# Kernel optimization log

Measured on AMD Instinct MI355X. Metric: run time of the kernel, lower is better.

## Reference

```python
import jax, jax.numpy as jnp
import numpy as np

N = 100000   # nodes
E = 1600000  # edges (avg degree 16)
DIN, DH, DOUT = 128, 64, 40


def setup_inputs() -> dict:
    key = jax.random.key(0)
    ks = jax.random.split(key, 6)
    x = jax.random.normal(ks[0], (N, DIN), dtype=jnp.float32)
    edge_index = jax.random.randint(ks[1], (2, E), 0, N, dtype=jnp.int32)
    s1 = float(1.0 / np.sqrt(DIN))
    s2 = float(1.0 / np.sqrt(DH))
    W1 = jax.random.uniform(ks[2], (DIN, DH), jnp.float32, -s1, s1)
    b1 = jax.random.uniform(ks[3], (DH,), jnp.float32, -s1, s1)
    W2 = jax.random.uniform(ks[4], (DH, DOUT), jnp.float32, -s2, s2)
    b2 = jax.random.uniform(ks[5], (DOUT,), jnp.float32, -s2, s2)
    return {"x": x, "W1": W1, "b1": b1, "W2": W2, "b2": b2, "edge_index": edge_index}


def _gcn_conv(x, W, b, src, dst):
    """PyG GCNConv: add self-loops, symmetric degree normalization, scatter-add."""
    n = x.shape[0]
    h = x @ W  # [N, F_out] — transform before propagation (PyG order)
    ones = jnp.ones(src.shape[0], dtype=h.dtype)
    deg = jax.ops.segment_sum(ones, dst, num_segments=n) + 1.0  # +1 for self-loop
    dinv = jax.lax.rsqrt(deg)  # deg >= 1, no zero guard needed
    norm = dinv[src] * dinv[dst]  # [E]
    agg = jax.ops.segment_sum(h[src] * norm[:, None], dst, num_segments=n)
    agg = agg + h * (dinv * dinv)[:, None]  # self-loop messages
    return agg + b


def reference(x, W1, b1, W2, b2, edge_index):
    src, dst = edge_index[0], edge_index[1]
    h = jax.nn.relu(_gcn_conv(x, W1, b1, src, dst))
    out = _gcn_conv(h, W2, b2, src, dst)
    return jax.nn.log_softmax(out, axis=1)
```

## Files before the change

kernel.cpp:

```cpp
#include <hip/hip_runtime.h>
#include <hip/hip_fp16.h>
#include <math.h>

#define N_NODES 100000
#define N_EDGES 1600000
#define DIN 128
#define DH 64
#define DOUT 40

#define NB 256
#define BN 391
#define CAP 8192
#define BIN_BLOCKS 512
#define EPB 3125

typedef unsigned short u16;
typedef unsigned int u32;

__device__ inline __half2 u2h(u32 u) {
    union { u32 x; __half2 h; } c; c.x = u; return c.h;
}
__device__ inline u32 h2u(__half2 h) {
    union { __half2 h; u32 x; } c; c.h = h; return c.x;
}


__global__ __launch_bounds__(256) void k_bin(const int* __restrict__ src,
                                             const int* __restrict__ dst,
                                             int* __restrict__ gcur,
                                             u32* __restrict__ staged) {
    __shared__ int hist[NB];
    __shared__ int base[NB];
    __shared__ int cur[NB];
    int t = threadIdx.x;
    for (int i = t; i < NB; i += 256) { hist[i] = 0; cur[i] = 0; }
    __syncthreads();
    int e0 = blockIdx.x * EPB;
    int e1 = e0 + EPB; if (e1 > N_EDGES) e1 = N_EDGES;
    for (int e = e0 + t; e < e1; e += 256)
        atomicAdd(&hist[dst[e] / BN], 1);
    __syncthreads();
    for (int i = t; i < NB; i += 256) {
        int h = hist[i];
        base[i] = h ? atomicAdd(&gcur[i], h) : 0;
    }
    __syncthreads();
    for (int e = e0 + t; e < e1; e += 256) {
        int d = dst[e], s = src[e];
        int b = d / BN;
        int dl = d - b * BN;
        int r = base[b] + atomicAdd(&cur[b], 1);
        if (r < CAP) staged[(size_t)b * CAP + r] = (u32)s | ((u32)dl << 17);
    }
}


__global__ __launch_bounds__(256) void k_csr(const int* __restrict__ gcur,
                                             const u32* __restrict__ staged,
                                             int* __restrict__ csr,
                                             int4* __restrict__ meta,
                                             float* __restrict__ dinv) {
    __shared__ u32 sedge[CAP];
    __shared__ int lcsr[CAP];
    __shared__ int hist[BN];
    __shared__ int lrs[BN];
    __shared__ int cur[BN];
    __shared__ int sbuf[256];
    int b = blockIdx.x, t = threadIdx.x;

    int part = 0;
    for (int i = t; i < b; i += 256) {
        int c = gcur[i]; if (c > CAP) c = CAP;
        part += c;
    }
    sbuf[t] = part;
    __syncthreads();
    for (int off = 128; off; off >>= 1) {
        if (t < off) sbuf[t] += sbuf[t + off];
        __syncthreads();
    }
    int base_ = sbuf[0];
    __syncthreads();

    int cnt = gcur[b]; if (cnt > CAP) cnt = CAP;
    for (int i = t; i < BN; i += 256) hist[i] = 0;
    for (int i = t; i < cnt; i += 256) sedge[i] = staged[(size_t)b * CAP + i];
    __syncthreads();
    for (int i = t; i < cnt; i += 256) atomicAdd(&hist[sedge[i] >> 17], 1);
    __syncthreads();

    int v0 = (2 * t < BN) ? hist[2 * t] : 0;
    int v1 = (2 * t + 1 < BN) ? hist[2 * t + 1] : 0;
    int s = v0 + v1;
    sbuf[t] = s;
    __syncthreads();
    for (int off = 1; off < 256; off <<= 1) {
        int add = (t >= off) ? sbuf[t - off] : 0;
        __syncthreads();
        sbuf[t] += add;
        __syncthreads();
    }
    int excl = sbuf[t] - s;
    if (2 * t < BN)     { lrs[2 * t] = excl;      cur[2 * t] = excl; }
    if (2 * t + 1 < BN) { lrs[2 * t + 1] = excl + v0; cur[2 * t + 1] = excl + v0; }
    __syncthreads();

    for (int i = t; i < cnt; i += 256) {
        u32 p = sedge[i];
        int pos = atomicAdd(&cur[p >> 17], 1);
        lcsr[pos] = (int)(p & 0x1FFFF);
    }
    __syncthreads();

    for (int i = t; i < cnt; i += 256) csr[base_ + i] = lcsr[i];
    int n0 = b * BN;
    for (int i = t; i < BN; i += 256) {
        int n = n0 + i;
        if (n < N_NODES) {
            int dg = hist[i];
            float dv = rsqrtf((float)dg + 1.0f);
            meta[n] = make_int4(base_ + lrs[i], dg, __float_as_int(dv), 0);
            dinv[n] = dv;
        }
    }
}


__global__ __launch_bounds__(256) void k_gemm1(const float* __restrict__ x,
                                               const float* __restrict__ W1,
                                               const float* __restrict__ dinv,
                                               u16* __restrict__ h1s) {
    __shared__ float xs[64 * 140];
    __shared__ float wsh[DIN * DH];
    int t = threadIdx.x;
    int row0 = blockIdx.x * 64;

    for (int it = 0; it < 8; ++it) {
        int idx = (it * 256 + t) * 4;
        int r = idx >> 7, c = idx & 127;
        float4 v = make_float4(0.f, 0.f, 0.f, 0.f);
        if (row0 + r < N_NODES) v = *(const float4*)&x[(size_t)(row0 + r) * DIN + c];
        *(float4*)&xs[r * 140 + c] = v;
    }
    for (int it = 0; it < 8; ++it) {
        int idx = (it * 256 + t) * 4;
        *(float4*)&wsh[idx] = *(const float4*)&W1[idx];
    }
    __syncthreads();

    int tr = t & 15;
    int tc = t >> 4;
    float acc[4][4] = {};
    for (int kb = 0; kb < DIN; kb += 4) {
        float4 w0 = *(const float4*)&wsh[(kb + 0) * DH + tr * 4];
        float4 w1 = *(const float4*)&wsh[(kb + 1) * DH + tr * 4];
        float4 w2 = *(const float4*)&wsh[(kb + 2) * DH + tr * 4];
        float4 w3 = *(const float4*)&wsh[(kb + 3) * DH + tr * 4];
#pragma unroll
        for (int i = 0; i < 4; ++i) {
            float4 xv = *(const float4*)&xs[(tc * 4 + i) * 140 + kb];
            acc[i][0] += xv.x * w0.x; acc[i][1] += xv.x * w0.y;
            acc[i][2] += xv.x * w0.z; acc[i][3] += xv.x * w0.w;
            acc[i][0] += xv.y * w1.x; acc[i][1] += xv.y * w1.y;
            acc[i][2] += xv.y * w1.z; acc[i][3] += xv.y * w1.w;
            acc[i][0] += xv.z * w2.x; acc[i][1] += xv.z * w2.y;
            acc[i][2] += xv.z * w2.z; acc[i][3] += xv.z * w2.w;
            acc[i][0] += xv.w * w3.x; acc[i][1] += xv.w * w3.y;
            acc[i][2] += xv.w * w3.z; acc[i][3] += xv.w * w3.w;
        }
    }
#pragma unroll
    for (int i = 0; i < 4; ++i) {
        int row = row0 + tc * 4 + i;
        if (row < N_NODES) {
            float dv = dinv[row];
            ushort4 o;
            o.x = __half_as_ushort(__float2half(acc[i][0] * dv));
            o.y = __half_as_ushort(__float2half(acc[i][1] * dv));
            o.z = __half_as_ushort(__float2half(acc[i][2] * dv));
            o.w = __half_as_ushort(__float2half(acc[i][3] * dv));
            *(ushort4*)&h1s[(size_t)row * DH + tr * 4] = o;
        }
    }
}


__global__ __launch_bounds__(256) void k_agg1(const u16* __restrict__ h1s,
                                              const int4* __restrict__ meta,
                                              const int* __restrict__ csr,
                                              const float* __restrict__ b1,
                                              float* __restrict__ h1) {
    int node = blockIdx.x * 4 + (threadIdx.x >> 6);
    if (node >= N_NODES) return;
    node = __builtin_amdgcn_readfirstlane(node);
    int lane = threadIdx.x & 63;
    int es = lane >> 4, fp = lane & 15;
    int4 me = meta[node];
    int s0 = me.x, d = me.y;
    float dv = __int_as_float(me.z);
    const uint2* rows = (const uint2*)h1s;
    __half2 A01 = __float2half2_rn(0.f), A23 = __float2half2_rn(0.f);
    if (es == 0) {
        uint2 v = rows[(u32)(node * 16 + fp)];
        A01 = u2h(v.x); A23 = u2h(v.y);
    }
    for (int base = 0; base < d; base += 64) {
        int nn = d - base; if (nn > 64) nn = 64;
        int myidx = (lane < nn) ? csr[s0 + base + lane] : 0;
        int j = 0;
        for (; j + 16 <= nn; j += 16) {
            int x0 = __builtin_amdgcn_ds_bpermute((j + es) * 4, myidx);
            int x1 = __builtin_amdgcn_ds_bpermute((j + 4 + es) * 4, myidx);
            int x2 = __builtin_amdgcn_ds_bpermute((j + 8 + es) * 4, myidx);
            int x3 = __builtin_amdgcn_ds_bpermute((j + 12 + es) * 4, myidx);
            uint2 v0 = rows[(u32)(x0 * 16 + fp)];
            uint2 v1 = rows[(u32)(x1 * 16 + fp)];
            uint2 v2 = rows[(u32)(x2 * 16 + fp)];
            uint2 v3 = rows[(u32)(x3 * 16 + fp)];
            A01 = __hadd2(A01, u2h(v0.x)); A23 = __hadd2(A23, u2h(v0.y));
            A01 = __hadd2(A01, u2h(v1.x)); A23 = __hadd2(A23, u2h(v1.y));
            A01 = __hadd2(A01, u2h(v2.x)); A23 = __hadd2(A23, u2h(v2.y));
            A01 = __hadd2(A01, u2h(v3.x)); A23 = __hadd2(A23, u2h(v3.y));
        }
        for (; j < nn; j += 4) {
            int x = __builtin_amdgcn_ds_bpermute((j + es) * 4, myidx);
            if (j + es < nn) {
                uint2 v = rows[(u32)(x * 16 + fp)];
                A01 = __hadd2(A01, u2h(v.x)); A23 = __hadd2(A23, u2h(v.y));
            }
        }
    }
    A01 = __hadd2(A01, u2h((u32)__shfl_xor((int)h2u(A01), 16, 64)));
    A23 = __hadd2(A23, u2h((u32)__shfl_xor((int)h2u(A23), 16, 64)));
    A01 = __hadd2(A01, u2h((u32)__shfl_xor((int)h2u(A01), 32, 64)));
    A23 = __hadd2(A23, u2h((u32)__shfl_xor((int)h2u(A23), 32, 64)));
    if (es == 0) {
        float4 bv = ((const float4*)b1)[fp];
        float4 o;
        o.x = fmaxf(__low2float(A01)  * dv + bv.x, 0.f);
        o.y = fmaxf(__high2float(A01) * dv + bv.y, 0.f);
        o.z = fmaxf(__low2float(A23)  * dv + bv.z, 0.f);
        o.w = fmaxf(__high2float(A23) * dv + bv.w, 0.f);
        ((float4*)h1)[(u32)(node * 16 + fp)] = o;
    }
}


__global__ __launch_bounds__(256) void k_gemm2(const float* __restrict__ h1,
                                               const float* __restrict__ W2,
                                               const float* __restrict__ dinv,
                                               u16* __restrict__ h2s) {
    __shared__ float xs[64 * 68];
    __shared__ float wsh[DH * DOUT];
    int t = threadIdx.x;
    int row0 = blockIdx.x * 64;

    for (int it = 0; it < 4; ++it) {
        int idx = (it * 256 + t) * 4;
        int r = idx >> 6, c = idx & 63;
        float4 v = make_float4(0.f, 0.f, 0.f, 0.f);
        if (row0 + r < N_NODES) v = *(const float4*)&h1[(size_t)(row0 + r) * DH + c];
        *(float4*)&xs[r * 68 + c] = v;
    }
    for (int idx = t * 4; idx < DH * DOUT; idx += 1024) {
        *(float4*)&wsh[idx] = *(const float4*)&W2[idx];
    }
    __syncthreads();

    int fg = t & 7;
    int rg = t >> 3;
    float acc[2][5] = {};
    for (int k = 0; k < DH; ++k) {
        float x0 = xs[(rg * 2 + 0) * 68 + k];
        float x1 = xs[(rg * 2 + 1) * 68 + k];
#pragma unroll
        for (int j = 0; j < 5; ++j) {
            float w = wsh[k * DOUT + fg * 5 + j];
            acc[0][j] += x0 * w;
            acc[1][j] += x1 * w;
        }
    }
#pragma unroll
    for (int i = 0; i < 2; ++i) {
        int row = row0 + rg * 2 + i;
        if (row < N_NODES) {
            float dvv = dinv[row];
#pragma unroll
            for (int j = 0; j < 5; ++j)
                h2s[(size_t)row * 64 + fg * 5 + j] =
                    __half_as_ushort(__float2half(acc[i][j] * dvv));
        }
    }
}


__global__ __launch_bounds__(256) void k_agg2(const u16* __restrict__ h2s,
                                              const int4* __restrict__ meta,
                                              const int* __restrict__ csr,
                                              const float* __restrict__ b2,
                                              float* __restrict__ out) {
    int node = blockIdx.x * 4 + (threadIdx.x >> 6);
    if (node >= N_NODES) return;
    node = __builtin_amdgcn_readfirstlane(node);
    int lane = threadIdx.x & 63;
    int es = lane >> 4, fp = lane & 15;
    bool act = fp < 10;
    int4 me = meta[node];
    int s0 = me.x, d = me.y;
    float dv = __int_as_float(me.z);
    const uint2* rows = (const uint2*)h2s;
    __half2 A01 = __float2half2_rn(0.f), A23 = __float2half2_rn(0.f);
    if (es == 0 && act) {
        uint2 v = rows[(u32)(node * 16 + fp)];
        A01 = u2h(v.x); A23 = u2h(v.y);
    }
    for (int base = 0; base < d; base += 64) {
        int nn = d - base; if (nn > 64) nn = 64;
        int myidx = (lane < nn) ? csr[s0 + base + lane] : 0;
        int j = 0;
        for (; j + 16 <= nn; j += 16) {
            int x0 = __builtin_amdgcn_ds_bpermute((j + es) * 4, myidx);
            int x1 = __builtin_amdgcn_ds_bpermute((j + 4 + es) * 4, myidx);
            int x2 = __builtin_amdgcn_ds_bpermute((j + 8 + es) * 4, myidx);
            int x3 = __builtin_amdgcn_ds_bpermute((j + 12 + es) * 4, myidx);
            if (act) {
                uint2 v0 = rows[(u32)(x0 * 16 + fp)];
                uint2 v1 = rows[(u32)(x1 * 16 + fp)];
                uint2 v2 = rows[(u32)(x2 * 16 + fp)];
                uint2 v3 = rows[(u32)(x3 * 16 + fp)];
                A01 = __hadd2(A01, u2h(v0.x)); A23 = __hadd2(A23, u2h(v0.y));
                A01 = __hadd2(A01, u2h(v1.x)); A23 = __hadd2(A23, u2h(v1.y));
                A01 = __hadd2(A01, u2h(v2.x)); A23 = __hadd2(A23, u2h(v2.y));
                A01 = __hadd2(A01, u2h(v3.x)); A23 = __hadd2(A23, u2h(v3.y));
            }
        }
        for (; j < nn; j += 4) {
            int x = __builtin_amdgcn_ds_bpermute((j + es) * 4, myidx);
            if (act && j + es < nn) {
                uint2 v = rows[(u32)(x * 16 + fp)];
                A01 = __hadd2(A01, u2h(v.x)); A23 = __hadd2(A23, u2h(v.y));
            }
        }
    }
    A01 = __hadd2(A01, u2h((u32)__shfl_xor((int)h2u(A01), 16, 64)));
    A23 = __hadd2(A23, u2h((u32)__shfl_xor((int)h2u(A23), 16, 64)));
    A01 = __hadd2(A01, u2h((u32)__shfl_xor((int)h2u(A01), 32, 64)));
    A23 = __hadd2(A23, u2h((u32)__shfl_xor((int)h2u(A23), 32, 64)));

    float4 bv = act ? ((const float4*)b2)[fp] : make_float4(0.f, 0.f, 0.f, 0.f);
    float v0 = act ? __low2float(A01)  * dv + bv.x : -INFINITY;
    float v1 = act ? __high2float(A01) * dv + bv.y : -INFINITY;
    float v2 = act ? __low2float(A23)  * dv + bv.z : -INFINITY;
    float v3 = act ? __high2float(A23) * dv + bv.w : -INFINITY;
    float m = fmaxf(fmaxf(v0, v1), fmaxf(v2, v3));
    m = fmaxf(m, __shfl_xor(m, 1, 64));
    m = fmaxf(m, __shfl_xor(m, 2, 64));
    m = fmaxf(m, __shfl_xor(m, 4, 64));
    m = fmaxf(m, __shfl_xor(m, 8, 64));
    float ex = act ? (expf(v0 - m) + expf(v1 - m) + expf(v2 - m) + expf(v3 - m)) : 0.f;
    ex += __shfl_xor(ex, 1, 64);
    ex += __shfl_xor(ex, 2, 64);
    ex += __shfl_xor(ex, 4, 64);
    ex += __shfl_xor(ex, 8, 64);
    float lse = m + logf(ex);
    if (es == 0 && act) {
        float4 o = make_float4(v0 - lse, v1 - lse, v2 - lse, v3 - lse);
        *(float4*)&out[(u32)(node * 40 + fp * 4)] = o;
    }
}


extern "C" void kernel_launch(void* const* d_in, const int* in_sizes, int n_in,
                              void* d_out, int out_size, void* d_ws, size_t ws_size,
                              hipStream_t stream) {
    const float* x  = (const float*)d_in[0];
    const float* W1 = (const float*)d_in[1];
    const float* b1 = (const float*)d_in[2];
    const float* W2 = (const float*)d_in[3];
    const float* b2 = (const float*)d_in[4];
    const int* eidx = (const int*)d_in[5];
    const int* srcp = eidx;
    const int* dstp = eidx + N_EDGES;
    float* out = (float*)d_out;

    char* w = (char*)d_ws;
    int* gcur    = (int*)w;   w += sizeof(int) * NB;
    float* dinv  = (float*)w; w += sizeof(float) * N_NODES + 48;
    int4* meta   = (int4*)w;  w += sizeof(int4) * N_NODES;
    u32* staged  = (u32*)w;   w += sizeof(u32) * (size_t)NB * CAP;
    int* csr     = (int*)w;   w += sizeof(int) * N_EDGES;
    u16* h1s     = (u16*)w;   w += sizeof(u16) * (size_t)N_NODES * DH;
    float* h1    = (float*)w; w += sizeof(float) * (size_t)N_NODES * DH;
    u16* h2s     = h1s;

    hipMemsetAsync(gcur, 0, sizeof(int) * NB, stream);
    k_bin<<<BIN_BLOCKS, 256, 0, stream>>>(srcp, dstp, gcur, staged);
    k_csr<<<NB, 256, 0, stream>>>(gcur, staged, csr, meta, dinv);
    k_gemm1<<<(N_NODES + 63) / 64, 256, 0, stream>>>(x, W1, dinv, h1s);
    k_agg1<<<(N_NODES + 3) / 4, 256, 0, stream>>>(h1s, meta, csr, b1, h1);
    k_gemm2<<<(N_NODES + 63) / 64, 256, 0, stream>>>(h1, W2, dinv, h2s);
    k_agg2<<<(N_NODES + 3) / 4, 256, 0, stream>>>(h2s, meta, csr, b2, out);
}
```

Baseline: 217.9 us.

## Widen aggregation gathers to 16-byte rows, 8 edges per wave step

Both aggregation kernels now have each lane load 16 bytes (8 halves) per neighbor row, so 8 lanes cover a 64-wide fp16 row and a wave handles 8 edges per step instead of 4. This halves the lane-index permutes per edge and uses wider loads. In layer 2 all 8 lanes load, so gemm2 now zeroes the padding columns 40..63 of h2s to keep those loads clean. The binning kernel also uses half as many blocks, each handling twice as many edges.

```diff
diff --git a/kernel.cpp b/kernel.cpp
--- a/kernel.cpp
+++ b/kernel.cpp
@@ -11,8 +11,8 @@
 #define NB 256
 #define BN 391
 #define CAP 8192
-#define BIN_BLOCKS 512
-#define EPB 3125
+#define BIN_BLOCKS 256
+#define EPB 6250
 
 typedef unsigned short u16;
 typedef unsigned int u32;
@@ -194,15 +194,15 @@
     if (node >= N_NODES) return;
     node = __builtin_amdgcn_readfirstlane(node);
     int lane = threadIdx.x & 63;
-    int es = lane >> 4, fp = lane & 15;
+    int es = lane >> 3, fq = lane & 7;
     int4 me = meta[node];
     int s0 = me.x, d = me.y;
     float dv = __int_as_float(me.z);
-    const uint2* rows = (const uint2*)h1s;
-    __half2 A01 = __float2half2_rn(0.f), A23 = __float2half2_rn(0.f);
+    const uint4* rows = (const uint4*)h1s;
+    __half2 A0 = __float2half2_rn(0.f), A1 = A0, A2 = A0, A3 = A0;
     if (es == 0) {
-        uint2 v = rows[(u32)(node * 16 + fp)];
-        A01 = u2h(v.x); A23 = u2h(v.y);
+        uint4 v = rows[(u32)(node * 8 + fq)];
+        A0 = u2h(v.x); A1 = u2h(v.y); A2 = u2h(v.z); A3 = u2h(v.w);
     }
     for (int base = 0; base < d; base += 64) {
         int nn = d - base; if (nn > 64) nn = 64;
@@ -210,38 +210,44 @@
         int j = 0;
         for (; j + 16 <= nn; j += 16) {
             int x0 = __builtin_amdgcn_ds_bpermute((j + es) * 4, myidx);
-            int x1 = __builtin_amdgcn_ds_bpermute((j + 4 + es) * 4, myidx);
-            int x2 = __builtin_amdgcn_ds_bpermute((j + 8 + es) * 4, myidx);
-            int x3 = __builtin_amdgcn_ds_bpermute((j + 12 + es) * 4, myidx);
-            uint2 v0 = rows[(u32)(x0 * 16 + fp)];
-            uint2 v1 = rows[(u32)(x1 * 16 + fp)];
-            uint2 v2 = rows[(u32)(x2 * 16 + fp)];
-            uint2 v3 = rows[(u32)(x3 * 16 + fp)];
-            A01 = __hadd2(A01, u2h(v0.x)); A23 = __hadd2(A23, u2h(v0.y));
-            A01 = __hadd2(A01, u2h(v1.x)); A23 = __hadd2(A23, u2h(v1.y));
-            A01 = __hadd2(A01, u2h(v2.x)); A23 = __hadd2(A23, u2h(v2.y));
-            A01 = __hadd2(A01, u2h(v3.x)); A23 = __hadd2(A23, u2h(v3.y));
-        }
-        for (; j < nn; j += 4) {
+            int x1 = __builtin_amdgcn_ds_bpermute((j + 8 + es) * 4, myidx);
+            uint4 v0 = rows[(u32)(x0 * 8 + fq)];
+            uint4 v1 = rows[(u32)(x1 * 8 + fq)];
+            A0 = __hadd2(A0, u2h(v0.x)); A1 = __hadd2(A1, u2h(v0.y));
+            A2 = __hadd2(A2, u2h(v0.z)); A3 = __hadd2(A3, u2h(v0.w));
+            A0 = __hadd2(A0, u2h(v1.x)); A1 = __hadd2(A1, u2h(v1.y));
+            A2 = __hadd2(A2, u2h(v1.z)); A3 = __hadd2(A3, u2h(v1.w));
+        }
+        for (; j < nn; j += 8) {
             int x = __builtin_amdgcn_ds_bpermute((j + es) * 4, myidx);
             if (j + es < nn) {
-                uint2 v = rows[(u32)(x * 16 + fp)];
-                A01 = __hadd2(A01, u2h(v.x)); A23 = __hadd2(A23, u2h(v.y));
+                uint4 v = rows[(u32)(x * 8 + fq)];
+                A0 = __hadd2(A0, u2h(v.x)); A1 = __hadd2(A1, u2h(v.y));
+                A2 = __hadd2(A2, u2h(v.z)); A3 = __hadd2(A3, u2h(v.w));
             }
         }
     }
-    A01 = __hadd2(A01, u2h((u32)__shfl_xor((int)h2u(A01), 16, 64)));
-    A23 = __hadd2(A23, u2h((u32)__shfl_xor((int)h2u(A23), 16, 64)));
-    A01 = __hadd2(A01, u2h((u32)__shfl_xor((int)h2u(A01), 32, 64)));
-    A23 = __hadd2(A23, u2h((u32)__shfl_xor((int)h2u(A23), 32, 64)));
+#pragma unroll
+    for (int off = 8; off <= 32; off <<= 1) {
+        A0 = __hadd2(A0, u2h((u32)__shfl_xor((int)h2u(A0), off, 64)));
+        A1 = __hadd2(A1, u2h((u32)__shfl_xor((int)h2u(A1), off, 64)));
+        A2 = __hadd2(A2, u2h((u32)__shfl_xor((int)h2u(A2), off, 64)));
+        A3 = __hadd2(A3, u2h((u32)__shfl_xor((int)h2u(A3), off, 64)));
+    }
     if (es == 0) {
-        float4 bv = ((const float4*)b1)[fp];
-        float4 o;
-        o.x = fmaxf(__low2float(A01)  * dv + bv.x, 0.f);
-        o.y = fmaxf(__high2float(A01) * dv + bv.y, 0.f);
-        o.z = fmaxf(__low2float(A23)  * dv + bv.z, 0.f);
-        o.w = fmaxf(__high2float(A23) * dv + bv.w, 0.f);
-        ((float4*)h1)[(u32)(node * 16 + fp)] = o;
+        float4 bva = ((const float4*)b1)[fq * 2 + 0];
+        float4 bvb = ((const float4*)b1)[fq * 2 + 1];
+        float4 oa, ob;
+        oa.x = fmaxf(__low2float(A0)  * dv + bva.x, 0.f);
+        oa.y = fmaxf(__high2float(A0) * dv + bva.y, 0.f);
+        oa.z = fmaxf(__low2float(A1)  * dv + bva.z, 0.f);
+        oa.w = fmaxf(__high2float(A1) * dv + bva.w, 0.f);
+        ob.x = fmaxf(__low2float(A2)  * dv + bvb.x, 0.f);
+        ob.y = fmaxf(__high2float(A2) * dv + bvb.y, 0.f);
+        ob.z = fmaxf(__low2float(A3)  * dv + bvb.z, 0.f);
+        ob.w = fmaxf(__high2float(A3) * dv + bvb.w, 0.f);
+        ((float4*)h1)[(u32)(node * 16 + fq * 2 + 0)] = oa;
+        ((float4*)h1)[(u32)(node * 16 + fq * 2 + 1)] = ob;
     }
 }
 
@@ -290,6 +296,12 @@
                 h2s[(size_t)row * 64 + fg * 5 + j] =
                     __half_as_ushort(__float2half(acc[i][j] * dvv));
         }
+    }
+    for (int i = t; i < 64 * 6; i += 256) {
+        int r = i / 6, c = i - r * 6;
+        int row = row0 + r;
+        if (row < N_NODES)
+            *(u32*)&h2s[(size_t)row * 64 + 40 + c * 4] = 0;
     }
 }
 
@@ -303,16 +315,16 @@
     if (node >= N_NODES) return;
     node = __builtin_amdgcn_readfirstlane(node);
     int lane = threadIdx.x & 63;
-    int es = lane >> 4, fp = lane & 15;
-    bool act = fp < 10;
+    int es = lane >> 3, fq = lane & 7;
+    bool act = fq < 5;
     int4 me = meta[node];
     int s0 = me.x, d = me.y;
     float dv = __int_as_float(me.z);
-    const uint2* rows = (const uint2*)h2s;
-    __half2 A01 = __float2half2_rn(0.f), A23 = __float2half2_rn(0.f);
-    if (es == 0 && act) {
-        uint2 v = rows[(u32)(node * 16 + fp)];
-        A01 = u2h(v.x); A23 = u2h(v.y);
+    const uint4* rows = (const uint4*)h2s;
+    __half2 A0 = __float2half2_rn(0.f), A1 = A0, A2 = A0, A3 = A0;
+    if (es == 0) {
+        uint4 v = rows[(u32)(node * 8 + fq)];
+        A0 = u2h(v.x); A1 = u2h(v.y); A2 = u2h(v.z); A3 = u2h(v.w);
     }
     for (int base = 0; base < d; base += 64) {
         int nn = d - base; if (nn > 64) nn = 64;
@@ -320,52 +332,60 @@
         int j = 0;
         for (; j + 16 <= nn; j += 16) {
             int x0 = __builtin_amdgcn_ds_bpermute((j + es) * 4, myidx);
-            int x1 = __builtin_amdgcn_ds_bpermute((j + 4 + es) * 4, myidx);
-            int x2 = __builtin_amdgcn_ds_bpermute((j + 8 + es) * 4, myidx);
-            int x3 = __builtin_amdgcn_ds_bpermute((j + 12 + es) * 4, myidx);
-            if (act) {
-                uint2 v0 = rows[(u32)(x0 * 16 + fp)];
-                uint2 v1 = rows[(u32)(x1 * 16 + fp)];
-                uint2 v2 = rows[(u32)(x2 * 16 + fp)];
-                uint2 v3 = rows[(u32)(x3 * 16 + fp)];
-                A01 = __hadd2(A01, u2h(v0.x)); A23 = __hadd2(A23, u2h(v0.y));
-                A01 = __hadd2(A01, u2h(v1.x)); A23 = __hadd2(A23, u2h(v1.y));
-                A01 = __hadd2(A01, u2h(v2.x)); A23 = __hadd2(A23, u2h(v2.y));
-                A01 = __hadd2(A01, u2h(v3.x)); A23 = __hadd2(A23, u2h(v3.y));
+            int x1 = __builtin_amdgcn_ds_bpermute((j + 8 + es) * 4, myidx);
+            uint4 v0 = rows[(u32)(x0 * 8 + fq)];
+            uint4 v1 = rows[(u32)(x1 * 8 + fq)];
+            A0 = __hadd2(A0, u2h(v0.x)); A1 = __hadd2(A1, u2h(v0.y));
+            A2 = __hadd2(A2, u2h(v0.z)); A3 = __hadd2(A3, u2h(v0.w));
+            A0 = __hadd2(A0, u2h(v1.x)); A1 = __hadd2(A1, u2h(v1.y));
+            A2 = __hadd2(A2, u2h(v1.z)); A3 = __hadd2(A3, u2h(v1.w));
+        }
+        for (; j < nn; j += 8) {
+            int x = __builtin_amdgcn_ds_bpermute((j + es) * 4, myidx);
+            if (j + es < nn) {
+                uint4 v = rows[(u32)(x * 8 + fq)];
+                A0 = __hadd2(A0, u2h(v.x)); A1 = __hadd2(A1, u2h(v.y));
+                A2 = __hadd2(A2, u2h(v.z)); A3 = __hadd2(A3, u2h(v.w));
             }
         }
-        for (; j < nn; j += 4) {
-            int x = __builtin_amdgcn_ds_bpermute((j + es) * 4, myidx);
-            if (act && j + es < nn) {
-                uint2 v = rows[(u32)(x * 16 + fp)];
-                A01 = __hadd2(A01, u2h(v.x)); A23 = __hadd2(A23, u2h(v.y));
-            }
-        }
-    }
-    A01 = __hadd2(A01, u2h((u32)__shfl_xor((int)h2u(A01), 16, 64)));
-    A23 = __hadd2(A23, u2h((u32)__shfl_xor((int)h2u(A23), 16, 64)));
-    A01 = __hadd2(A01, u2h((u32)__shfl_xor((int)h2u(A01), 32, 64)));
-    A23 = __hadd2(A23, u2h((u32)__shfl_xor((int)h2u(A23), 32, 64)));
-
-    float4 bv = act ? ((const float4*)b2)[fp] : make_float4(0.f, 0.f, 0.f, 0.f);
-    float v0 = act ? __low2float(A01)  * dv + bv.x : -INFINITY;
-    float v1 = act ? __high2float(A01) * dv + bv.y : -INFINITY;
-    float v2 = act ? __low2float(A23)  * dv + bv.z : -INFINITY;
-    float v3 = act ? __high2float(A23) * dv + bv.w : -INFINITY;
-    float m = fmaxf(fmaxf(v0, v1), fmaxf(v2, v3));
+    }
+#pragma unroll
+    for (int off = 8; off <= 32; off <<= 1) {
+        A0 = __hadd2(A0, u2h((u32)__shfl_xor((int)h2u(A0), off, 64)));
+        A1 = __hadd2(A1, u2h((u32)__shfl_xor((int)h2u(A1), off, 64)));
+        A2 = __hadd2(A2, u2h((u32)__shfl_xor((int)h2u(A2), off, 64)));
+        A3 = __hadd2(A3, u2h((u32)__shfl_xor((int)h2u(A3), off, 64)));
+    }
+
+    float4 bva = act ? ((const float4*)b2)[fq * 2 + 0] : make_float4(0.f, 0.f, 0.f, 0.f);
+    float4 bvb = act ? ((const float4*)b2)[fq * 2 + 1] : make_float4(0.f, 0.f, 0.f, 0.f);
+    float v0 = act ? __low2float(A0)  * dv + bva.x : -INFINITY;
+    float v1 = act ? __high2float(A0) * dv + bva.y : -INFINITY;
+    float v2 = act ? __low2float(A1)  * dv + bva.z : -INFINITY;
+    float v3 = act ? __high2float(A1) * dv + bva.w : -INFINITY;
+    float v4 = act ? __low2float(A2)  * dv + bvb.x : -INFINITY;
+    float v5 = act ? __high2float(A2) * dv + bvb.y : -INFINITY;
+    float v6 = act ? __low2float(A3)  * dv + bvb.z : -INFINITY;
+    float v7 = act ? __high2float(A3) * dv + bvb.w : -INFINITY;
+    float m = fmaxf(fmaxf(fmaxf(v0, v1), fmaxf(v2, v3)),
+                    fmaxf(fmaxf(v4, v5), fmaxf(v6, v7)));
     m = fmaxf(m, __shfl_xor(m, 1, 64));
     m = fmaxf(m, __shfl_xor(m, 2, 64));
     m = fmaxf(m, __shfl_xor(m, 4, 64));
-    m = fmaxf(m, __shfl_xor(m, 8, 64));
-    float ex = act ? (expf(v0 - m) + expf(v1 - m) + expf(v2 - m) + expf(v3 - m)) : 0.f;
+    float ex = 0.f;
+    if (act) {
+        ex = expf(v0 - m) + expf(v1 - m) + expf(v2 - m) + expf(v3 - m)
+           + expf(v4 - m) + expf(v5 - m) + expf(v6 - m) + expf(v7 - m);
+    }
     ex += __shfl_xor(ex, 1, 64);
     ex += __shfl_xor(ex, 2, 64);
     ex += __shfl_xor(ex, 4, 64);
-    ex += __shfl_xor(ex, 8, 64);
     float lse = m + logf(ex);
     if (es == 0 && act) {
-        float4 o = make_float4(v0 - lse, v1 - lse, v2 - lse, v3 - lse);
-        *(float4*)&out[(u32)(node * 40 + fp * 4)] = o;
+        float4 oa = make_float4(v0 - lse, v1 - lse, v2 - lse, v3 - lse);
+        float4 ob = make_float4(v4 - lse, v5 - lse, v6 - lse, v7 - lse);
+        *(float4*)&out[(u32)(node * 40 + fq * 8 + 0)] = oa;
+        *(float4*)&out[(u32)(node * 40 + fq * 8 + 4)] = ob;
     }
 }
 
```

After: 223.7 us. 2.7% more time.
